# Optimization experiments

Hardware: AMD Instinct MI355X
Metric: run time of the kernel (lower is better)

The kernel has to match this reference:

```python
import jax, jax.numpy as jnp
import numpy as np

EPS = 1e-5  # torch BatchNorm1d default eps


def _batchnorm(x, gamma, beta):
    # training-mode BatchNorm1d: biased batch statistics over the N dim
    mean = jnp.mean(x, axis=0)
    var = jnp.var(x, axis=0)
    return (x - mean) * jax.lax.rsqrt(var + EPS) * gamma + beta


def setup_inputs() -> dict:
    key = jax.random.key(0)
    ks = jax.random.split(key, 12)
    N_last, N_cur, E, F = 100000, 50000, 500000, 300
    Din = F + 3  # 303: neighbor features concat coord delta
    inp = {
        "last_coors": jax.random.normal(ks[0], (N_last, 3), jnp.float32),
        "last_features": jax.random.normal(ks[1], (N_last, F), jnp.float32),
        "current_coors": jax.random.normal(ks[2], (N_cur, 3), jnp.float32),
        "cur_idx": jax.random.randint(ks[3], (E,), 0, N_cur),
        "last_idx": jax.random.randint(ks[4], (E,), 0, N_last),
        # in_linear: Linear(303,300) + ReLU + BN(300)
        "W1": jax.random.normal(ks[5], (Din, F), jnp.float32) / np.sqrt(Din),
        "b1": jnp.zeros((F,), jnp.float32),
        "g1": jnp.ones((F,), jnp.float32),
        "be1": jnp.zeros((F,), jnp.float32),
        # out_linear: Linear(300,300) + ReLU + BN(300)
        "W2": jax.random.normal(ks[6], (F, F), jnp.float32) / np.sqrt(F),
        "b2": jnp.zeros((F,), jnp.float32),
        "g2": jnp.ones((F,), jnp.float32),
        "be2": jnp.zeros((F,), jnp.float32),
    }
    return inp


def reference(last_coors, last_features, current_coors, cur_idx, last_idx,
              W1, b1, g1, be1, W2, b2, g2, be2):
    N_cur = current_coors.shape[0]
    # gather: neighbor features + (neighbor - center) coordinate deltas -> [E, 303]
    edge_feats = jnp.concatenate(
        [last_features[last_idx], last_coors[last_idx] - current_coors[cur_idx]],
        axis=1)
    # in_linear MLP on edges
    h = _batchnorm(jnp.maximum(edge_feats @ W1 + b1, 0.0), g1, be1)  # [E, 300]
    # scatter-max aggregation to current-level nodes (empty segments -> 0,
    # matching torch_scatter.scatter(..., reduce='max') zero-init behavior)
    agg = jax.ops.segment_max(h, cur_idx, num_segments=N_cur)  # [N_cur, 300]
    agg = jnp.where(jnp.isfinite(agg), agg, 0.0)
    # out_linear MLP on nodes
    out = _batchnorm(jnp.maximum(agg @ W2 + b2, 0.0), g2, be2)
    return out
```

## Files before the change

kernel.cpp:

```cpp
#include <hip/hip_runtime.h>
#include <hip/hip_bf16.h>


#define NPART 64
#define SB 256
#define SEGB 32
#define CHS 256
#define UNR 8

typedef __bf16 bf16_t;
typedef __bf16 bf16x4 __attribute__((ext_vector_type(4)));
typedef __bf16 bf16x8 __attribute__((ext_vector_type(8)));
typedef float f32x4 __attribute__((ext_vector_type(4)));

__device__ __forceinline__ unsigned enc_f32(float x) {
    unsigned u = __float_as_uint(x);
    return (u & 0x80000000u) ? ~u : (u | 0x80000000u);
}
__device__ __forceinline__ float dec_f32(unsigned e) {
    unsigned u = (e & 0x80000000u) ? (e & 0x7fffffffu) : ~e;
    return __uint_as_float(u);
}

__global__ void hist_k(const int* __restrict__ ci, int E, int* __restrict__ hist)
{
    const int e = blockIdx.x * 256 + threadIdx.x;
    if (e < E) atomicAdd(&hist[ci[e]], 1);
}

__global__ void scan_reduce(const int* __restrict__ hist, int nseg, int* __restrict__ bsum)
{
    __shared__ int s[SB];
    const int tid = threadIdx.x;
    const int i = blockIdx.x * SB + tid;
    s[tid] = (i < nseg) ? hist[i] : 0;
    __syncthreads();
    for (int o = SB / 2; o > 0; o >>= 1) {
        if (tid < o) s[tid] += s[tid + o];
        __syncthreads();
    }
    if (tid == 0) bsum[blockIdx.x] = s[0];
}

__global__ void scan_top(int* __restrict__ bsum, int nb)
{
    __shared__ int s[SB];
    const int tid = threadIdx.x;
    const int v = (tid < nb) ? bsum[tid] : 0;
    s[tid] = v;
    __syncthreads();
    for (int o = 1; o < SB; o <<= 1) {
        int x = 0;
        if (tid >= o) x = s[tid - o];
        __syncthreads();
        s[tid] += x;
        __syncthreads();
    }
    if (tid < nb) bsum[tid] = s[tid] - v;
}

__global__ void scan_final(const int* __restrict__ hist, int nseg,
                           const int* __restrict__ bsum, int* __restrict__ cnt)
{
    __shared__ int s[SB];
    const int tid = threadIdx.x;
    const int i = blockIdx.x * SB + tid;
    const int v = (i < nseg) ? hist[i] : 0;
    s[tid] = v;
    __syncthreads();
    for (int o = 1; o < SB; o <<= 1) {
        int x = 0;
        if (tid >= o) x = s[tid - o];
        __syncthreads();
        s[tid] += x;
        __syncthreads();
    }
    if (i < nseg) cnt[i] = s[tid] - v + bsum[blockIdx.x];
}

__global__ void scatter_k(const int* __restrict__ ci, const int* __restrict__ li,
                          int E, int* __restrict__ cnt, int2* __restrict__ sorted)
{
    const int e = blockIdx.x * 256 + threadIdx.x;
    if (e >= E) return;
    const int c = ci[e];
    const int pos = atomicAdd(&cnt[c], 1);
    sorted[pos] = make_int2(li[e], c);
}

__global__ void pack_wt(const float* __restrict__ W, bf16_t* __restrict__ WT)
{
    const int idx = blockIdx.x * 256 + threadIdx.x;
    if (idx >= 384 * 320) return;
    const int n = idx / 320, k = idx % 320;
    float v = (n < 300 && k < 300) ? W[k * 300 + n] : 0.f;
    WT[idx] = (bf16_t)v;
}

__global__ void cvt_lf(const float* __restrict__ lf, bf16_t* __restrict__ out, int M)
{
    const int idx = blockIdx.x * 256 + threadIdx.x;
    const int r = idx / 40, c8 = (idx % 40) * 8;
    if (r >= M) return;
    bf16x8 v = {};
    if (c8 + 8 <= 300) {
        const float4 a = *reinterpret_cast<const float4*>(&lf[(long)r * 300 + c8]);
        const float4 b = *reinterpret_cast<const float4*>(&lf[(long)r * 300 + c8 + 4]);
        v = (bf16x8){(bf16_t)a.x, (bf16_t)a.y, (bf16_t)a.z, (bf16_t)a.w,
                     (bf16_t)b.x, (bf16_t)b.y, (bf16_t)b.z, (bf16_t)b.w};
    } else if (c8 < 300) {
        const float4 a = *reinterpret_cast<const float4*>(&lf[(long)r * 300 + c8]);
        v[0] = (bf16_t)a.x; v[1] = (bf16_t)a.y; v[2] = (bf16_t)a.z; v[3] = (bf16_t)a.w;
    }
    *reinterpret_cast<bf16x8*>(&out[(long)r * 320 + c8]) = v;
}

template<int MODE>
__launch_bounds__(256)
__global__ void gemm_mfma(const bf16_t* __restrict__ A, int M,
                          const bf16_t* __restrict__ WT,
                          const float* __restrict__ bias,
                          bf16_t* __restrict__ outBF,
                          float* __restrict__ outF,
                          float* __restrict__ part)
{
    __shared__ bf16_t As[128][72];
    __shared__ bf16_t Bs[160][72];
    __shared__ float sSum[160], sSq[160];

    const int tid  = threadIdx.x;
    const int lane = tid & 63, wv = tid >> 6;
    const int wm = wv & 1, wn = wv >> 1;
    const int m0 = blockIdx.x * 128, n0 = blockIdx.y * 160;
    const int rl = lane & 15, quad = lane >> 4;

    if (MODE == 1 && tid < 160) { sSum[tid] = 0.f; sSq[tid] = 0.f; }

    f32x4 acc[4][5];
    #pragma unroll
    for (int i = 0; i < 4; ++i)
        #pragma unroll
        for (int j = 0; j < 5; ++j)
            acc[i][j] = (f32x4){0.f, 0.f, 0.f, 0.f};

    for (int k0 = 0; k0 < 320; k0 += 64) {
        #pragma unroll
        for (int i = 0; i < 4; ++i) {
            const int id = i * 256 + tid;
            const int r = id >> 3, kc = (id & 7) * 8;
            const int gr = min(m0 + r, M - 1);
            bf16x8 a8 = *reinterpret_cast<const bf16x8*>(&A[(long)gr * 320 + k0 + kc]);
            *reinterpret_cast<bf16x8*>(&As[r][kc]) = a8;
        }
        #pragma unroll
        for (int i = 0; i < 5; ++i) {
            const int id = i * 256 + tid;
            const int n = id >> 3, kc = (id & 7) * 8;
            bf16x8 w8 = *reinterpret_cast<const bf16x8*>(&WT[(long)(n0 + n) * 320 + k0 + kc]);
            *reinterpret_cast<bf16x8*>(&Bs[n][kc]) = w8;
        }
        __syncthreads();

        #pragma unroll
        for (int kk = 0; kk < 2; ++kk) {
            const int kb = kk * 32 + quad * 8;
            bf16x8 af[4], bfr[5];
            #pragma unroll
            for (int mi = 0; mi < 4; ++mi)
                af[mi] = *reinterpret_cast<const bf16x8*>(&As[wm * 64 + mi * 16 + rl][kb]);
            #pragma unroll
            for (int nj = 0; nj < 5; ++nj)
                bfr[nj] = *reinterpret_cast<const bf16x8*>(&Bs[wn * 80 + nj * 16 + rl][kb]);
            #pragma unroll
            for (int mi = 0; mi < 4; ++mi)
                #pragma unroll
                for (int nj = 0; nj < 5; ++nj)
                    acc[mi][nj] = __builtin_amdgcn_mfma_f32_16x16x32_bf16(
                        af[mi], bfr[nj], acc[mi][nj], 0, 0, 0);
        }
        __syncthreads();
    }

    if (MODE == 0) {
        #pragma unroll
        for (int mi = 0; mi < 4; ++mi)
            #pragma unroll
            for (int nj = 0; nj < 5; ++nj)
                #pragma unroll
                for (int reg = 0; reg < 4; ++reg) {
                    const int r = m0 + wm * 64 + mi * 16 + quad * 4 + reg;
                    const int c = n0 + wn * 80 + nj * 16 + rl;
                    if (r < M) {
                        const float v = (c < 300) ? (acc[mi][nj][reg] + bias[c]) : 0.f;
                        outBF[(long)r * 320 + c] = (bf16_t)v;
                    }
                }
    } else {
        float csum[5] = {}, csq[5] = {};
        #pragma unroll
        for (int mi = 0; mi < 4; ++mi)
            #pragma unroll
            for (int nj = 0; nj < 5; ++nj)
                #pragma unroll
                for (int reg = 0; reg < 4; ++reg) {
                    const int r = m0 + wm * 64 + mi * 16 + quad * 4 + reg;
                    const int c = n0 + wn * 80 + nj * 16 + rl;
                    if (r < M && c < 300) {
                        float v = fmaxf(acc[mi][nj][reg] + bias[c], 0.f);
                        outF[(long)r * 300 + c] = v;
                        csum[nj] += v; csq[nj] += v * v;
                    }
                }
        #pragma unroll
        for (int nj = 0; nj < 5; ++nj) {
            const int cl = wn * 80 + nj * 16 + rl;
            atomicAdd(&sSum[cl], csum[nj]);
            atomicAdd(&sSq[cl], csq[nj]);
        }
        __syncthreads();
        const int slot = (blockIdx.x + blockIdx.y * gridDim.x) & (NPART - 1);
        if (tid < 160 && (n0 + tid) < 300) {
            atomicAdd(&part[slot * 600 + n0 + tid], sSum[tid]);
            atomicAdd(&part[slot * 600 + 300 + n0 + tid], sSq[tid]);
        }
    }
}

__launch_bounds__(320)
__global__ void edge_pass(const bf16_t* __restrict__ Gb,
                          const float* __restrict__ last_coors,
                          const float* __restrict__ cur_coors,
                          const int2* __restrict__ sorted,
                          const int*  __restrict__ segEnd,
                          const float* __restrict__ Wc,
                          const float* __restrict__ g1,
                          unsigned* __restrict__ zbuf,
                          float* __restrict__ part1,
                          int N_cur)
{
    __shared__ int sRow[2][CHS], sCi[2][CHS];
    __shared__ float sD0[2][CHS], sD1[2][CHS], sD2[2][CHS];

    const int tid = threadIdx.x;
    const int st  = (tid >= 160) ? 1 : 0;
    const int ts  = tid - st * 160;

    const int g0   = blockIdx.x * SEGB;
    const int gEnd = min(g0 + SEGB, N_cur);
    const int gMid = min(g0 + SEGB / 2, gEnd);

    const int e00 = (g0   == 0) ? 0 : segEnd[g0 - 1];
    const int e01 = (gMid == 0) ? 0 : segEnd[gMid - 1];
    const int e11 = (gEnd == 0) ? 0 : segEnd[gEnd - 1];

    const int ebeg = st ? e01 : e00;
    const int eend = st ? e11 : e01;

    const int nch0 = (e01 - e00 + CHS - 1) / CHS;
    const int nch1 = (e11 - e01 + CHS - 1) / CHS;
    const int nch  = max(nch0, nch1);

    const int ft = ts * 2;
    const bool real = (ft < 300);
    float w00 = 0.f, w01 = 0.f, w10 = 0.f, w11 = 0.f, w20 = 0.f, w21 = 0.f;
    float sgn0 = 1.f, sgn1 = 1.f;
    if (real) {
        w00 = Wc[ft];        w01 = Wc[ft + 1];
        w10 = Wc[300 + ft];  w11 = Wc[300 + ft + 1];
        w20 = Wc[600 + ft];  w21 = Wc[600 + ft + 1];
        sgn0 = (g1[ft]     < 0.f) ? -1.f : 1.f;
        sgn1 = (g1[ft + 1] < 0.f) ? -1.f : 1.f;
    }

    int cur = -1;
    float m0 = -3.4e38f, m1 = -3.4e38f;
    float sum0 = 0.f, sq0 = 0.f, sum1 = 0.f, sq1 = 0.f;

    for (int ch = 0; ch < nch; ++ch) {
        const int cbeg = ebeg + ch * CHS;
        const int ccnt = min(CHS, eend - cbeg);

        for (int i = ts; i < ccnt; i += 160) {
            const int2 r = sorted[cbeg + i];
            sRow[st][i] = r.x * 320;
            sCi[st][i]  = r.y;
            sD0[st][i] = last_coors[r.x * 3 + 0] - cur_coors[r.y * 3 + 0];
            sD1[st][i] = last_coors[r.x * 3 + 1] - cur_coors[r.y * 3 + 1];
            sD2[st][i] = last_coors[r.x * 3 + 2] - cur_coors[r.y * 3 + 2];
        }
        __syncthreads();

        int i = 0;
        for (; i + UNR <= ccnt; i += UNR) {
            unsigned gu[UNR];
            #pragma unroll
            for (int j = 0; j < UNR; ++j)
                gu[j] = *reinterpret_cast<const unsigned*>(&Gb[(long)sRow[st][i + j] + ft]);
            #pragma unroll
            for (int j = 0; j < UNR; ++j) {
                const int ci = sCi[st][i + j];
                if (ci != cur) {
                    if (cur >= 0) {
                        zbuf[(long)cur * 320 + ft]     = enc_f32(m0);
                        zbuf[(long)cur * 320 + ft + 1] = enc_f32(m1);
                    }
                    cur = ci;
                    m0 = -3.4e38f; m1 = -3.4e38f;
                }
                const float gx = __uint_as_float(gu[j] << 16);
                const float gy = __uint_as_float(gu[j] & 0xffff0000u);
                const float d0 = sD0[st][i + j], d1 = sD1[st][i + j], d2 = sD2[st][i + j];
                const float y0 = fmaxf(gx + d0 * w00 + d1 * w10 + d2 * w20, 0.f);
                const float y1 = fmaxf(gy + d0 * w01 + d1 * w11 + d2 * w21, 0.f);
                sum0 += y0; sq0 += y0 * y0; m0 = fmaxf(m0, sgn0 * y0);
                sum1 += y1; sq1 += y1 * y1; m1 = fmaxf(m1, sgn1 * y1);
            }
        }
        for (; i < ccnt; ++i) {
            const int ci = sCi[st][i];
            if (ci != cur) {
                if (cur >= 0) {
                    zbuf[(long)cur * 320 + ft]     = enc_f32(m0);
                    zbuf[(long)cur * 320 + ft + 1] = enc_f32(m1);
                }
                cur = ci;
                m0 = -3.4e38f; m1 = -3.4e38f;
            }
            const unsigned gu = *reinterpret_cast<const unsigned*>(&Gb[(long)sRow[st][i] + ft]);
            const float gx = __uint_as_float(gu << 16);
            const float gy = __uint_as_float(gu & 0xffff0000u);
            const float d0 = sD0[st][i], d1 = sD1[st][i], d2 = sD2[st][i];
            const float y0 = fmaxf(gx + d0 * w00 + d1 * w10 + d2 * w20, 0.f);
            const float y1 = fmaxf(gy + d0 * w01 + d1 * w11 + d2 * w21, 0.f);
            sum0 += y0; sq0 += y0 * y0; m0 = fmaxf(m0, sgn0 * y0);
            sum1 += y1; sq1 += y1 * y1; m1 = fmaxf(m1, sgn1 * y1);
        }
        __syncthreads();
    }
    if (cur >= 0) {
        zbuf[(long)cur * 320 + ft]     = enc_f32(m0);
        zbuf[(long)cur * 320 + ft + 1] = enc_f32(m1);
    }

    const int slot = blockIdx.x & (NPART - 1);
    if (real) {
        atomicAdd(&part1[slot * 600 + ft],           sum0);
        atomicAdd(&part1[slot * 600 + ft + 1],       sum1);
        atomicAdd(&part1[slot * 600 + 300 + ft],     sq0);
        atomicAdd(&part1[slot * 600 + 300 + ft + 1], sq1);
    }
}

__global__ void stats_finalize(const float* __restrict__ part,
                               const float* __restrict__ g,
                               const float* __restrict__ be,
                               float invCnt, float* __restrict__ ac)
{
    const int t = threadIdx.x;
    if (t >= 300) return;
    float sum = 0.f, sq = 0.f;
    for (int p = 0; p < NPART; ++p) {
        sum += part[p * 600 + t];
        sq  += part[p * 600 + 300 + t];
    }
    const float mean = sum * invCnt;
    const float var = fmaxf(sq * invCnt - mean * mean, 0.f);
    const float inv = rsqrtf(var + 1e-5f);
    const float a = g[t] * inv;
    ac[t] = a;
    ac[300 + t] = be[t] - mean * a;
}

__global__ void agg_finalize(const unsigned* __restrict__ zbuf,
                             const float* __restrict__ ac1,
                             bf16_t* __restrict__ Ab2)
{
    const int t = threadIdx.x;
    float v = 0.f;
    if (t < 300) {
        const unsigned u = zbuf[(long)blockIdx.x * 320 + t];
        if (u != 0u) v = fabsf(ac1[t]) * dec_f32(u) + ac1[300 + t];
    }
    Ab2[(long)blockIdx.x * 320 + t] = (bf16_t)v;
}

__global__ void finalize_out(float* __restrict__ out,
                             const float* __restrict__ ac2)
{
    const int t = threadIdx.x;
    if (t >= 300) return;
    const long i = (long)blockIdx.x * 300 + t;
    out[i] = ac2[t] * out[i] + ac2[300 + t];
}

extern "C" void kernel_launch(void* const* d_in, const int* in_sizes, int n_in,
                              void* d_out, int out_size, void* d_ws, size_t ws_size,
                              hipStream_t stream)
{
    const float* last_coors    = (const float*)d_in[0];
    const float* last_features = (const float*)d_in[1];
    const float* cur_coors     = (const float*)d_in[2];
    const int*   cur_idx       = (const int*)d_in[3];
    const int*   last_idx      = (const int*)d_in[4];
    const float* W1  = (const float*)d_in[5];
    const float* b1  = (const float*)d_in[6];
    const float* g1  = (const float*)d_in[7];
    const float* be1 = (const float*)d_in[8];
    const float* W2  = (const float*)d_in[9];
    const float* b2  = (const float*)d_in[10];
    const float* g2  = (const float*)d_in[11];
    const float* be2 = (const float*)d_in[12];
    float* out = (float*)d_out;

    const int N_last = in_sizes[0] / 3;
    const int N_cur  = in_sizes[2] / 3;
    const int E      = in_sizes[3];

    const int nb1 = (N_cur + SB - 1) / SB;

    char* ws = (char*)d_ws;
    size_t off = 0;
    const size_t sz_r0 = (size_t)N_last * 320 * 2;
    bf16_t* Gb  = (bf16_t*)(ws + off);
    bf16_t* Ab2 = (bf16_t*)(ws + off);
    off += sz_r0; off = (off + 255) & ~(size_t)255;
    const size_t sz_alf = (size_t)N_last * 320 * 2;
    const size_t sz_zb  = (size_t)N_cur * 320 * 4;
    bf16_t* Alf = (bf16_t*)(ws + off);
    unsigned* zbuf = (unsigned*)(ws + off);
    off += (sz_alf > sz_zb ? sz_alf : sz_zb); off = (off + 255) & ~(size_t)255;
    int2* sorted = (int2*)(ws + off);  off += (size_t)E * 8;
    int* hist = (int*)(ws + off);      off += (size_t)nb1 * SB * 4;
    int* cnt  = (int*)(ws + off);      off += (size_t)nb1 * SB * 4;
    int* bsum = (int*)(ws + off);      off += 256 * 4;
    bf16_t* WT1 = (bf16_t*)(ws + off); off += (size_t)384 * 320 * 2;
    bf16_t* WT2 = (bf16_t*)(ws + off); off += (size_t)384 * 320 * 2;
    float* part1 = (float*)(ws + off); off += (size_t)NPART * 600 * 4;
    float* part2 = (float*)(ws + off); off += (size_t)NPART * 600 * 4;
    float* ac1   = (float*)(ws + off); off += 600 * 4;
    float* ac2   = (float*)(ws + off); off += 600 * 4;

    hipMemsetAsync(hist, 0, (size_t)nb1 * SB * 4, stream);
    hipMemsetAsync(part1, 0, (size_t)NPART * 600 * 4, stream);
    hipMemsetAsync(part2, 0, (size_t)NPART * 600 * 4, stream);

    hist_k<<<(E + 255) / 256, 256, 0, stream>>>(cur_idx, E, hist);
    scan_reduce<<<nb1, SB, 0, stream>>>(hist, N_cur, bsum);
    scan_top<<<1, SB, 0, stream>>>(bsum, nb1);
    scan_final<<<nb1, SB, 0, stream>>>(hist, N_cur, bsum, cnt);
    scatter_k<<<(E + 255) / 256, 256, 0, stream>>>(cur_idx, last_idx, E, cnt, sorted);

    pack_wt<<<480, 256, 0, stream>>>(W1, WT1);
    pack_wt<<<480, 256, 0, stream>>>(W2, WT2);
    cvt_lf<<<((N_last * 40) + 255) / 256, 256, 0, stream>>>(last_features, Alf, N_last);

    dim3 gridG((N_last + 127) / 128, 2);
    gemm_mfma<0><<<gridG, 256, 0, stream>>>(Alf, N_last, WT1, b1, Gb, nullptr, nullptr);

    hipMemsetAsync(zbuf, 0, sz_zb, stream);

    const int nSB = (N_cur + SEGB - 1) / SEGB;
    edge_pass<<<nSB, 320, 0, stream>>>(Gb, last_coors, cur_coors, sorted, cnt,
                                       W1 + 300 * 300, g1, zbuf, part1, N_cur);

    stats_finalize<<<1, 320, 0, stream>>>(part1, g1, be1, 1.0f / (float)E, ac1);
    agg_finalize<<<N_cur, 320, 0, stream>>>(zbuf, ac1, Ab2);

    dim3 grid2((N_cur + 127) / 128, 2);
    gemm_mfma<1><<<grid2, 256, 0, stream>>>(Ab2, N_cur, WT2, b2, nullptr, out, part2);

    stats_finalize<<<1, 320, 0, stream>>>(part2, g2, be2, 1.0f / (float)N_cur, ac2);
    finalize_out<<<N_cur, 320, 0, stream>>>(out, ac2);
}
```

Before: 586.3 us.

## Fuse fp32-to-bf16 conversion and agg finalize into GEMM A-tile loads

The separate last_features conversion kernel is removed, and the first GEMM now reads fp32 rows and converts them to bf16 while loading the A tile. The agg_finalize pass is folded into the second GEMM's A-load: it reads raw fp32 max values, applies the BN1 affine, and zeros empty segments by checking segment counts. The zbuf memset and the order-preserving encoding are dropped because empty segments are now detected from segEnd. The two weight-pack launches and two memsets are merged. This removes intermediate buffer round-trips and several launches, at the cost of heavier and less vectorised A-tile loads inside both GEMMs.

```diff
diff --git a/kernel.cpp b/kernel.cpp
--- a/kernel.cpp
+++ b/kernel.cpp
@@ -9,18 +9,8 @@
 #define UNR 8
 
 typedef __bf16 bf16_t;
-typedef __bf16 bf16x4 __attribute__((ext_vector_type(4)));
 typedef __bf16 bf16x8 __attribute__((ext_vector_type(8)));
 typedef float f32x4 __attribute__((ext_vector_type(4)));
-
-__device__ __forceinline__ unsigned enc_f32(float x) {
-    unsigned u = __float_as_uint(x);
-    return (u & 0x80000000u) ? ~u : (u | 0x80000000u);
-}
-__device__ __forceinline__ float dec_f32(unsigned e) {
-    unsigned u = (e & 0x80000000u) ? (e & 0x7fffffffu) : ~e;
-    return __uint_as_float(u);
-}
 
 __global__ void hist_k(const int* __restrict__ ci, int E, int* __restrict__ hist)
 {
@@ -88,36 +78,24 @@
     sorted[pos] = make_int2(li[e], c);
 }
 
-__global__ void pack_wt(const float* __restrict__ W, bf16_t* __restrict__ WT)
+__global__ void pack_wt2(const float* __restrict__ W1, const float* __restrict__ W2,
+                         bf16_t* __restrict__ WT)
 {
     const int idx = blockIdx.x * 256 + threadIdx.x;
-    if (idx >= 384 * 320) return;
-    const int n = idx / 320, k = idx % 320;
+    if (idx >= 2 * 384 * 320) return;
+    const int w = idx / (384 * 320);
+    const int rem = idx - w * (384 * 320);
+    const int n = rem / 320, k = rem % 320;
+    const float* W = w ? W2 : W1;
     float v = (n < 300 && k < 300) ? W[k * 300 + n] : 0.f;
     WT[idx] = (bf16_t)v;
 }
 
-__global__ void cvt_lf(const float* __restrict__ lf, bf16_t* __restrict__ out, int M)
-{
-    const int idx = blockIdx.x * 256 + threadIdx.x;
-    const int r = idx / 40, c8 = (idx % 40) * 8;
-    if (r >= M) return;
-    bf16x8 v = {};
-    if (c8 + 8 <= 300) {
-        const float4 a = *reinterpret_cast<const float4*>(&lf[(long)r * 300 + c8]);
-        const float4 b = *reinterpret_cast<const float4*>(&lf[(long)r * 300 + c8 + 4]);
-        v = (bf16x8){(bf16_t)a.x, (bf16_t)a.y, (bf16_t)a.z, (bf16_t)a.w,
-                     (bf16_t)b.x, (bf16_t)b.y, (bf16_t)b.z, (bf16_t)b.w};
-    } else if (c8 < 300) {
-        const float4 a = *reinterpret_cast<const float4*>(&lf[(long)r * 300 + c8]);
-        v[0] = (bf16_t)a.x; v[1] = (bf16_t)a.y; v[2] = (bf16_t)a.z; v[3] = (bf16_t)a.w;
-    }
-    *reinterpret_cast<bf16x8*>(&out[(long)r * 320 + c8]) = v;
-}
-
 template<int MODE>
 __launch_bounds__(256)
-__global__ void gemm_mfma(const bf16_t* __restrict__ A, int M,
+__global__ void gemm_mfma(const float* __restrict__ A32, int M,
+                          const int* __restrict__ segEnd,
+                          const float* __restrict__ ac,
                           const bf16_t* __restrict__ WT,
                           const float* __restrict__ bias,
                           bf16_t* __restrict__ outBF,
@@ -149,8 +127,39 @@
             const int id = i * 256 + tid;
             const int r = id >> 3, kc = (id & 7) * 8;
             const int gr = min(m0 + r, M - 1);
-            bf16x8 a8 = *reinterpret_cast<const bf16x8*>(&A[(long)gr * 320 + k0 + kc]);
-            *reinterpret_cast<bf16x8*>(&As[r][kc]) = a8;
+            const int c0 = k0 + kc;
+            bf16x8 v = {};
+            if (MODE == 0) {
+                if (c0 + 8 <= 300) {
+                    const float4 a = *reinterpret_cast<const float4*>(&A32[(long)gr * 300 + c0]);
+                    const float4 b = *reinterpret_cast<const float4*>(&A32[(long)gr * 300 + c0 + 4]);
+                    v = (bf16x8){(bf16_t)a.x, (bf16_t)a.y, (bf16_t)a.z, (bf16_t)a.w,
+                                 (bf16_t)b.x, (bf16_t)b.y, (bf16_t)b.z, (bf16_t)b.w};
+                } else if (c0 < 300) {
+                    const float4 a = *reinterpret_cast<const float4*>(&A32[(long)gr * 300 + c0]);
+                    v[0] = (bf16_t)a.x; v[1] = (bf16_t)a.y;
+                    v[2] = (bf16_t)a.z; v[3] = (bf16_t)a.w;
+                }
+            } else {
+                const bool emp = segEnd[gr] == (gr ? segEnd[gr - 1] : 0);
+                const float4 ma = *reinterpret_cast<const float4*>(&A32[(long)gr * 320 + c0]);
+                const float4 mb = *reinterpret_cast<const float4*>(&A32[(long)gr * 320 + c0 + 4]);
+                const float4 aa = *reinterpret_cast<const float4*>(&ac[c0]);
+                const float4 ab = *reinterpret_cast<const float4*>(&ac[c0 + 4]);
+                const float4 ca = *reinterpret_cast<const float4*>(&ac[320 + c0]);
+                const float4 cb = *reinterpret_cast<const float4*>(&ac[320 + c0 + 4]);
+                const float t0 = emp ? 0.f : fabsf(aa.x) * ma.x + ca.x;
+                const float t1 = emp ? 0.f : fabsf(aa.y) * ma.y + ca.y;
+                const float t2 = emp ? 0.f : fabsf(aa.z) * ma.z + ca.z;
+                const float t3 = emp ? 0.f : fabsf(aa.w) * ma.w + ca.w;
+                const float t4 = emp ? 0.f : fabsf(ab.x) * mb.x + cb.x;
+                const float t5 = emp ? 0.f : fabsf(ab.y) * mb.y + cb.y;
+                const float t6 = emp ? 0.f : fabsf(ab.z) * mb.z + cb.z;
+                const float t7 = emp ? 0.f : fabsf(ab.w) * mb.w + cb.w;
+                v = (bf16x8){(bf16_t)t0, (bf16_t)t1, (bf16_t)t2, (bf16_t)t3,
+                             (bf16_t)t4, (bf16_t)t5, (bf16_t)t6, (bf16_t)t7};
+            }
+            *reinterpret_cast<bf16x8*>(&As[r][kc]) = v;
         }
         #pragma unroll
         for (int i = 0; i < 5; ++i) {
@@ -234,7 +243,7 @@
                           const int*  __restrict__ segEnd,
                           const float* __restrict__ Wc,
                           const float* __restrict__ g1,
-                          unsigned* __restrict__ zbuf,
+                          float* __restrict__ zbuf,
                           float* __restrict__ part1,
                           int N_cur)
 {
@@ -300,10 +309,9 @@
             for (int j = 0; j < UNR; ++j) {
                 const int ci = sCi[st][i + j];
                 if (ci != cur) {
-                    if (cur >= 0) {
-                        zbuf[(long)cur * 320 + ft]     = enc_f32(m0);
-                        zbuf[(long)cur * 320 + ft + 1] = enc_f32(m1);
-                    }
+                    if (cur >= 0)
+                        *reinterpret_cast<float2*>(&zbuf[(long)cur * 320 + ft]) =
+                            make_float2(m0, m1);
                     cur = ci;
                     m0 = -3.4e38f; m1 = -3.4e38f;
                 }
@@ -319,10 +327,9 @@
         for (; i < ccnt; ++i) {
             const int ci = sCi[st][i];
             if (ci != cur) {
-                if (cur >= 0) {
-                    zbuf[(long)cur * 320 + ft]     = enc_f32(m0);
-                    zbuf[(long)cur * 320 + ft + 1] = enc_f32(m1);
-                }
+                if (cur >= 0)
+                    *reinterpret_cast<float2*>(&zbuf[(long)cur * 320 + ft]) =
+                        make_float2(m0, m1);
                 cur = ci;
                 m0 = -3.4e38f; m1 = -3.4e38f;
             }
@@ -337,10 +344,8 @@
         }
         __syncthreads();
     }
-    if (cur >= 0) {
-        zbuf[(long)cur * 320 + ft]     = enc_f32(m0);
-        zbuf[(long)cur * 320 + ft + 1] = enc_f32(m1);
-    }
+    if (cur >= 0)
+        *reinterpret_cast<float2*>(&zbuf[(long)cur * 320 + ft]) = make_float2(m0, m1);
 
     const int slot = blockIdx.x & (NPART - 1);
     if (real) {
@@ -357,7 +362,10 @@
                                float invCnt, float* __restrict__ ac)
 {
     const int t = threadIdx.x;
-    if (t >= 300) return;
+    if (t >= 300) {
+        if (t < 320) { ac[t] = 0.f; ac[320 + t] = 0.f; }
+        return;
+    }
     float sum = 0.f, sq = 0.f;
     for (int p = 0; p < NPART; ++p) {
         sum += part[p * 600 + t];
@@ -368,20 +376,7 @@
     const float inv = rsqrtf(var + 1e-5f);
     const float a = g[t] * inv;
     ac[t] = a;
-    ac[300 + t] = be[t] - mean * a;
-}
-
-__global__ void agg_finalize(const unsigned* __restrict__ zbuf,
-                             const float* __restrict__ ac1,
-                             bf16_t* __restrict__ Ab2)
-{
-    const int t = threadIdx.x;
-    float v = 0.f;
-    if (t < 300) {
-        const unsigned u = zbuf[(long)blockIdx.x * 320 + t];
-        if (u != 0u) v = fabsf(ac1[t]) * dec_f32(u) + ac1[300 + t];
-    }
-    Ab2[(long)blockIdx.x * 320 + t] = (bf16_t)v;
+    ac[320 + t] = be[t] - mean * a;
 }
 
 __global__ void finalize_out(float* __restrict__ out,
@@ -390,7 +385,7 @@
     const int t = threadIdx.x;
     if (t >= 300) return;
     const long i = (long)blockIdx.x * 300 + t;
-    out[i] = ac2[t] * out[i] + ac2[300 + t];
+    out[i] = ac2[t] * out[i] + ac2[320 + t];
 }
 
 extern "C" void kernel_launch(void* const* d_in, const int* in_sizes, int n_in,
@@ -420,15 +415,10 @@
 
     char* ws = (char*)d_ws;
     size_t off = 0;
-    const size_t sz_r0 = (size_t)N_last * 320 * 2;
-    bf16_t* Gb  = (bf16_t*)(ws + off);
-    bf16_t* Ab2 = (bf16_t*)(ws + off);
-    off += sz_r0; off = (off + 255) & ~(size_t)255;
-    const size_t sz_alf = (size_t)N_last * 320 * 2;
-    const size_t sz_zb  = (size_t)N_cur * 320 * 4;
-    bf16_t* Alf = (bf16_t*)(ws + off);
-    unsigned* zbuf = (unsigned*)(ws + off);
-    off += (sz_alf > sz_zb ? sz_alf : sz_zb); off = (off + 255) & ~(size_t)255;
+    bf16_t* Gb = (bf16_t*)(ws + off);  off += (size_t)N_last * 320 * 2;
+    off = (off + 255) & ~(size_t)255;
+    float* zbuf = (float*)(ws + off);  off += (size_t)N_cur * 320 * 4;
+    off = (off + 255) & ~(size_t)255;
     int2* sorted = (int2*)(ws + off);  off += (size_t)E * 8;
     int* hist = (int*)(ws + off);      off += (size_t)nb1 * SB * 4;
     int* cnt  = (int*)(ws + off);      off += (size_t)nb1 * SB * 4;
@@ -437,12 +427,11 @@
     bf16_t* WT2 = (bf16_t*)(ws + off); off += (size_t)384 * 320 * 2;
     float* part1 = (float*)(ws + off); off += (size_t)NPART * 600 * 4;
     float* part2 = (float*)(ws + off); off += (size_t)NPART * 600 * 4;
-    float* ac1   = (float*)(ws + off); off += 600 * 4;
-    float* ac2   = (float*)(ws + off); off += 600 * 4;
+    float* ac1   = (float*)(ws + off); off += 640 * 4;
+    float* ac2   = (float*)(ws + off); off += 640 * 4;
 
     hipMemsetAsync(hist, 0, (size_t)nb1 * SB * 4, stream);
-    hipMemsetAsync(part1, 0, (size_t)NPART * 600 * 4, stream);
-    hipMemsetAsync(part2, 0, (size_t)NPART * 600 * 4, stream);
+    hipMemsetAsync(part1, 0, (size_t)2 * NPART * 600 * 4, stream);
 
     hist_k<<<(E + 255) / 256, 256, 0, stream>>>(cur_idx, E, hist);
     scan_reduce<<<nb1, SB, 0, stream>>>(hist, N_cur, bsum);
@@ -450,24 +439,21 @@
     scan_final<<<nb1, SB, 0, stream>>>(hist, N_cur, bsum, cnt);
     scatter_k<<<(E + 255) / 256, 256, 0, stream>>>(cur_idx, last_idx, E, cnt, sorted);
 
-    pack_wt<<<480, 256, 0, stream>>>(W1, WT1);
-    pack_wt<<<480, 256, 0, stream>>>(W2, WT2);
-    cvt_lf<<<((N_last * 40) + 255) / 256, 256, 0, stream>>>(last_features, Alf, N_last);
+    pack_wt2<<<960, 256, 0, stream>>>(W1, W2, WT1);
 
     dim3 gridG((N_last + 127) / 128, 2);
-    gemm_mfma<0><<<gridG, 256, 0, stream>>>(Alf, N_last, WT1, b1, Gb, nullptr, nullptr);
-
-    hipMemsetAsync(zbuf, 0, sz_zb, stream);
+    gemm_mfma<0><<<gridG, 256, 0, stream>>>(last_features, N_last, nullptr, nullptr,
+                                            WT1, b1, Gb, nullptr, nullptr);
 
     const int nSB = (N_cur + SEGB - 1) / SEGB;
     edge_pass<<<nSB, 320, 0, stream>>>(Gb, last_coors, cur_coors, sorted, cnt,
                                        W1 + 300 * 300, g1, zbuf, part1, N_cur);
 
     stats_finalize<<<1, 320, 0, stream>>>(part1, g1, be1, 1.0f / (float)E, ac1);
-    agg_finalize<<<N_cur, 320, 0, stream>>>(zbuf, ac1, Ab2);
 
     dim3 grid2((N_cur + 127) / 128, 2);
-    gemm_mfma<1><<<grid2, 256, 0, stream>>>(Ab2, N_cur, WT2, b2, nullptr, out, part2);
+    gemm_mfma<1><<<grid2, 256, 0, stream>>>(zbuf, N_cur, cnt, ac1,
+                                            WT2, b2, nullptr, out, part2);
 
     stats_finalize<<<1, 320, 0, stream>>>(part2, g2, be2, 1.0f / (float)N_cur, ac2);
     finalize_out<<<N_cur, 320, 0, stream>>>(out, ac2);
```

After: 587.9 us. No clear change (+0.3%).
